# Optimization experiments

Measured on AMD Instinct MI355X. Metric: run time of the kernel, lower is better.

Reference implementation:

```python
import jax, jax.numpy as jnp
import numpy as np

MASK_SIZE = 28
IMG_H, IMG_W = 520, 704
NUM_GT = 128
NUM_PROP = 512


def box_iou(a, b):
    # a: [P,4], b: [G,4] in xyxy -> [P,G]
    area_a = (a[:, 2] - a[:, 0]) * (a[:, 3] - a[:, 1])
    area_b = (b[:, 2] - b[:, 0]) * (b[:, 3] - b[:, 1])
    lt = jnp.maximum(a[:, None, :2], b[None, :, :2])
    rb = jnp.minimum(a[:, None, 2:], b[None, :, 2:])
    wh = jnp.clip(rb - lt, 0.0)
    inter = wh[..., 0] * wh[..., 1]
    return inter / (area_a[:, None] + area_b[None, :] - inter)


def crop_resize_one(box, gidx, gt_masks):
    # Faithful to extract_mask_target: int-truncate box, clamp, crop, bilinear
    # resize (align_corners=False) to MASK_SIZE x MASK_SIZE.
    S = MASK_SIZE
    H, W = gt_masks.shape[1], gt_masks.shape[2]
    x1 = jnp.clip(box[0].astype(jnp.int32), 0, W - 1)
    y1 = jnp.clip(box[1].astype(jnp.int32), 0, H - 1)
    x2 = jnp.maximum(x1 + 1, jnp.minimum(box[2].astype(jnp.int32), W))
    y2 = jnp.maximum(y1 + 1, jnp.minimum(box[3].astype(jnp.int32), H))
    cwi = x2 - x1
    chi = y2 - y1
    cw = cwi.astype(jnp.float32)
    ch = chi.astype(jnp.float32)
    j = jnp.arange(S, dtype=jnp.float32)
    # source coords inside crop, border-clamped (PyTorch bilinear, align_corners=False)
    sx = jnp.clip((j + 0.5) * cw / S - 0.5, 0.0, cw - 1.0)
    sy = jnp.clip((j + 0.5) * ch / S - 0.5, 0.0, ch - 1.0)
    x0 = jnp.floor(sx)
    y0 = jnp.floor(sy)
    wx = sx - x0
    wy = sy - y0
    x0i = x0.astype(jnp.int32)
    y0i = y0.astype(jnp.int32)
    x1i = jnp.minimum(x0i + 1, cwi - 1)
    y1i = jnp.minimum(y0i + 1, chi - 1)
    m = gt_masks[gidx]  # [H, W]
    ax0 = x0i + x1
    ax1 = x1i + x1
    ay0 = y0i + y1
    ay1 = y1i + y1
    v00 = m[ay0[:, None], ax0[None, :]]
    v01 = m[ay0[:, None], ax1[None, :]]
    v10 = m[ay1[:, None], ax0[None, :]]
    v11 = m[ay1[:, None], ax1[None, :]]
    top = (1.0 - wx)[None, :] * v00 + wx[None, :] * v01
    bot = (1.0 - wx)[None, :] * v10 + wx[None, :] * v11
    return (1.0 - wy)[:, None] * top + wy[:, None] * bot  # [S, S]


def setup_inputs() -> dict:
    key = jax.random.key(0)
    k1, k2, k3, k4, k5 = jax.random.split(key, 5)
    # GT boxes: cell-like boxes inside a 520x704 image
    cx = jax.random.uniform(k1, (NUM_GT,), minval=50.0, maxval=IMG_W - 50.0)
    cy = jax.random.uniform(k2, (NUM_GT,), minval=50.0, maxval=IMG_H - 50.0)
    wh = jax.random.uniform(k3, (NUM_GT, 2), minval=20.0, maxval=80.0)
    gt_boxes = jnp.stack([cx - wh[:, 0] / 2, cy - wh[:, 1] / 2,
                          cx + wh[:, 0] / 2, cy + wh[:, 1] / 2], axis=1)
    # proposals: jittered copies of GT boxes -> realistic positive fraction
    reps = NUM_PROP // NUM_GT
    noise = jax.random.normal(k4, (NUM_PROP, 4)) * 4.0
    proposals = jnp.tile(gt_boxes, (reps, 1)) + noise
    # per-instance binary masks (float, as .float() in the torch code)
    gt_masks = (jax.random.uniform(k5, (NUM_GT, IMG_H, IMG_W)) < 0.3).astype(jnp.float32)
    mask_logits = jax.random.normal(jax.random.fold_in(key, 7),
                                    (NUM_PROP, 2, MASK_SIZE, MASK_SIZE), dtype=jnp.float32)
    return {"proposals": proposals, "gt_boxes": gt_boxes,
            "gt_masks": gt_masks, "mask_logits": mask_logits}


def reference(proposals, gt_boxes, gt_masks, mask_logits):
    S = MASK_SIZE
    ious = box_iou(proposals, gt_boxes)           # [P, G]
    max_ious = ious.max(axis=1)
    matched = jnp.argmax(ious, axis=1)            # [P]
    pos = (max_ious > 0.5).astype(jnp.float32)    # [P]
    matched_boxes = gt_boxes[matched]             # [P, 4]
    # batched crop + bilinear resize of matched GT masks (RoI-style gather)
    targets = jax.vmap(crop_resize_one, in_axes=(0, 0, None))(matched_boxes, matched, gt_masks)  # [P,S,S]
    logits = mask_logits[:, 1]                    # foreground channel [P,S,S]
    # stable BCE with logits
    bce = jnp.maximum(logits, 0.0) - logits * targets + jnp.log1p(jnp.exp(-jnp.abs(logits)))
    npos = pos.sum()
    loss_pos = jnp.sum(bce * pos[:, None, None]) / (jnp.maximum(npos, 1.0) * S * S)
    loss_neg = jnp.mean(mask_logits ** 2) * 0.01
    return jnp.where(npos > 0, loss_pos, loss_neg)
```

## Files before the change

kernel.cpp:

```cpp
#include <hip/hip_runtime.h>
#include <math.h>

#define NUM_GT   128
#define NUM_PROP 512
#define IMG_H    520
#define IMG_W    704
#define MS       28
#define LOGITS_N (NUM_PROP * 2 * MS * MS)

#define WS_MATCHED_OFF 256
#define WS_POS_OFF     (256 + NUM_PROP * 4)
#define WS_ZERO_BYTES  (256 + NUM_PROP * 8)

__global__ void match_kernel(const float* __restrict__ proposals,
                             const float* __restrict__ gt_boxes,
                             int* __restrict__ matched,
                             float* __restrict__ pos,
                             float* __restrict__ npos) {
    __shared__ float gb[NUM_GT * 4];
    for (int i = threadIdx.x; i < NUM_GT * 4; i += blockDim.x) gb[i] = gt_boxes[i];
    __syncthreads();

    int p = blockIdx.x * blockDim.x + threadIdx.x;
    if (p >= NUM_PROP) return;

    float ax1 = proposals[p * 4 + 0];
    float ay1 = proposals[p * 4 + 1];
    float ax2 = proposals[p * 4 + 2];
    float ay2 = proposals[p * 4 + 3];
    float area_a = (ax2 - ax1) * (ay2 - ay1);

    float best = -1e30f;
    int bi = 0;
    for (int g = 0; g < NUM_GT; ++g) {
        float bx1 = gb[g * 4 + 0];
        float by1 = gb[g * 4 + 1];
        float bx2 = gb[g * 4 + 2];
        float by2 = gb[g * 4 + 3];
        float area_b = (bx2 - bx1) * (by2 - by1);
        float ltx = fmaxf(ax1, bx1), lty = fmaxf(ay1, by1);
        float rbx = fminf(ax2, bx2), rby = fminf(ay2, by2);
        float w = fmaxf(rbx - ltx, 0.0f);
        float h = fmaxf(rby - lty, 0.0f);
        float inter = w * h;
        float iou = inter / (area_a + area_b - inter);
        if (iou > best) { best = iou; bi = g; }
    }
    matched[p] = bi;
    float ps = (best > 0.5f) ? 1.0f : 0.0f;
    pos[p] = ps;
    atomicAdd(npos, ps);
}

__global__ void bce_kernel(const float* __restrict__ gt_boxes,
                           const float* __restrict__ gt_masks,
                           const float* __restrict__ mask_logits,
                           const int* __restrict__ matched,
                           const float* __restrict__ pos,
                           float* __restrict__ bce_sum) {
    const int p = blockIdx.x;
    const int t = threadIdx.x;

    __shared__ int   s_gidx;
    __shared__ int   s_x0[MS], s_x1[MS], s_y0[MS], s_y1[MS];
    __shared__ float s_wx[MS], s_wy[MS];
    __shared__ float red[4];

    if (t == 0) s_gidx = matched[p];
    __syncthreads();
    const int g = s_gidx;

    const float b0 = gt_boxes[g * 4 + 0];
    const float b1 = gt_boxes[g * 4 + 1];
    const float b2 = gt_boxes[g * 4 + 2];
    const float b3 = gt_boxes[g * 4 + 3];

    int x1 = min(max((int)b0, 0), IMG_W - 1);
    int y1 = min(max((int)b1, 0), IMG_H - 1);
    int x2 = max(x1 + 1, min((int)b2, IMG_W));
    int y2 = max(y1 + 1, min((int)b3, IMG_H));
    int cwi = x2 - x1;
    int chi = y2 - y1;
    float cw = (float)cwi;
    float ch = (float)chi;

    if (t < MS) {
        float j = (float)t + 0.5f;
        float sx = fminf(fmaxf(j * cw / 28.0f - 0.5f, 0.0f), cw - 1.0f);
        float x0f = floorf(sx);
        int x0i = (int)x0f;
        s_wx[t] = sx - x0f;
        s_x0[t] = x0i + x1;
        s_x1[t] = min(x0i + 1, cwi - 1) + x1;

        float sy = fminf(fmaxf(j * ch / 28.0f - 0.5f, 0.0f), ch - 1.0f);
        float y0f = floorf(sy);
        int y0i = (int)y0f;
        s_wy[t] = sy - y0f;
        s_y0[t] = y0i + y1;
        s_y1[t] = min(y0i + 1, chi - 1) + y1;
    }
    __syncthreads();

    const float* m  = gt_masks + (size_t)g * IMG_H * IMG_W;
    const float* lg = mask_logits + ((size_t)p * 2 + 1) * (MS * MS);

    float acc = 0.0f;
    for (int idx = t; idx < MS * MS; idx += blockDim.x) {
        int i = idx / MS;
        int j = idx - i * MS;
        float wx = s_wx[j], wy = s_wy[i];
        const float* r0 = m + (size_t)s_y0[i] * IMG_W;
        const float* r1 = m + (size_t)s_y1[i] * IMG_W;
        int cx0 = s_x0[j], cx1 = s_x1[j];
        float v00 = r0[cx0], v01 = r0[cx1];
        float v10 = r1[cx0], v11 = r1[cx1];
        float top = (1.0f - wx) * v00 + wx * v01;
        float bot = (1.0f - wx) * v10 + wx * v11;
        float tv  = (1.0f - wy) * top + wy * bot;
        float l = lg[idx];
        float bce = fmaxf(l, 0.0f) - l * tv + log1pf(expf(-fabsf(l)));
        acc += bce;
    }

    float v = acc;
    #pragma unroll
    for (int o = 32; o > 0; o >>= 1) v += __shfl_down(v, o, 64);
    int lane = t & 63, wid = t >> 6;
    if (lane == 0) red[wid] = v;
    __syncthreads();
    if (t == 0) {
        float s = red[0] + red[1] + red[2] + red[3];
        atomicAdd(bce_sum, s * pos[p]);
    }
}

__global__ void sq_kernel(const float* __restrict__ mask_logits,
                          float* __restrict__ sqsum) {
    const int nvec = LOGITS_N / 4;
    const float4* src = (const float4*)mask_logits;
    float acc = 0.0f;
    for (int i = blockIdx.x * blockDim.x + threadIdx.x; i < nvec;
         i += gridDim.x * blockDim.x) {
        float4 x = src[i];
        acc += x.x * x.x + x.y * x.y + x.z * x.z + x.w * x.w;
    }
    float v = acc;
    #pragma unroll
    for (int o = 32; o > 0; o >>= 1) v += __shfl_down(v, o, 64);
    __shared__ float red[4];
    int lane = threadIdx.x & 63, wid = threadIdx.x >> 6;
    if (lane == 0) red[wid] = v;
    __syncthreads();
    if (threadIdx.x == 0) {
        float s = red[0] + red[1] + red[2] + red[3];
        atomicAdd(sqsum, s);
    }
}

__global__ void final_kernel(const float* __restrict__ acc, float* __restrict__ out) {
    float bce  = acc[0];
    float npos = acc[1];
    float sq   = acc[2];
    float loss_pos = bce / (fmaxf(npos, 1.0f) * (float)(MS * MS));
    float loss_neg = (sq / (float)LOGITS_N) * 0.01f;
    out[0] = (npos > 0.0f) ? loss_pos : loss_neg;
}

extern "C" void kernel_launch(void* const* d_in, const int* in_sizes, int n_in,
                              void* d_out, int out_size, void* d_ws, size_t ws_size,
                              hipStream_t stream) {
    const float* proposals   = (const float*)d_in[0];
    const float* gt_boxes    = (const float*)d_in[1];
    const float* gt_masks    = (const float*)d_in[2];
    const float* mask_logits = (const float*)d_in[3];
    float* out = (float*)d_out;

    float* acc     = (float*)d_ws;
    int*   matched = (int*)((char*)d_ws + WS_MATCHED_OFF);
    float* pos     = (float*)((char*)d_ws + WS_POS_OFF);

    hipMemsetAsync(d_ws, 0, WS_ZERO_BYTES, stream);

    match_kernel<<<(NUM_PROP + 255) / 256, 256, 0, stream>>>(proposals, gt_boxes,
                                                             matched, pos, acc + 1);
    bce_kernel<<<NUM_PROP, 256, 0, stream>>>(gt_boxes, gt_masks, mask_logits,
                                             matched, pos, acc + 0);
    sq_kernel<<<128, 256, 0, stream>>>(mask_logits, acc + 2);
    final_kernel<<<1, 1, 0, stream>>>(acc, out);
}
```

Before: 249.9 us.

## Fuse matching, BCE, square-sum and finalize into one kernel with last-block reduction

Merges the four kernels and the memset into a single launch. Each proposal block computes its IoU argmax cooperatively in shared memory, skips the mask gather and BCE for non-positive proposals, and extra blocks compute the squared-logit sum. The last block to finish, found through an atomic counter, writes the loss and resets the device-global accumulators. This removes launch overhead and the memset, at the cost of relying on global state reset between calls and a fence-based completion protocol.

```diff
diff --git a/kernel.cpp b/kernel.cpp
--- a/kernel.cpp
+++ b/kernel.cpp
@@ -7,185 +7,180 @@
 #define IMG_W    704
 #define MS       28
 #define LOGITS_N (NUM_PROP * 2 * MS * MS)
+#define SQ_BLOCKS 128
+#define TOTAL_BLOCKS (NUM_PROP + SQ_BLOCKS)
 
-#define WS_MATCHED_OFF 256
-#define WS_POS_OFF     (256 + NUM_PROP * 4)
-#define WS_ZERO_BYTES  (256 + NUM_PROP * 8)
+__device__ float    g_bce  = 0.0f;
+__device__ float    g_npos = 0.0f;
+__device__ float    g_sq   = 0.0f;
+__device__ unsigned g_done = 0u;
 
-__global__ void match_kernel(const float* __restrict__ proposals,
-                             const float* __restrict__ gt_boxes,
-                             int* __restrict__ matched,
-                             float* __restrict__ pos,
-                             float* __restrict__ npos) {
-    __shared__ float gb[NUM_GT * 4];
-    for (int i = threadIdx.x; i < NUM_GT * 4; i += blockDim.x) gb[i] = gt_boxes[i];
-    __syncthreads();
-
-    int p = blockIdx.x * blockDim.x + threadIdx.x;
-    if (p >= NUM_PROP) return;
-
-    float ax1 = proposals[p * 4 + 0];
-    float ay1 = proposals[p * 4 + 1];
-    float ax2 = proposals[p * 4 + 2];
-    float ay2 = proposals[p * 4 + 3];
-    float area_a = (ax2 - ax1) * (ay2 - ay1);
-
-    float best = -1e30f;
-    int bi = 0;
-    for (int g = 0; g < NUM_GT; ++g) {
-        float bx1 = gb[g * 4 + 0];
-        float by1 = gb[g * 4 + 1];
-        float bx2 = gb[g * 4 + 2];
-        float by2 = gb[g * 4 + 3];
-        float area_b = (bx2 - bx1) * (by2 - by1);
-        float ltx = fmaxf(ax1, bx1), lty = fmaxf(ay1, by1);
-        float rbx = fminf(ax2, bx2), rby = fminf(ay2, by2);
-        float w = fmaxf(rbx - ltx, 0.0f);
-        float h = fmaxf(rby - lty, 0.0f);
-        float inter = w * h;
-        float iou = inter / (area_a + area_b - inter);
-        if (iou > best) { best = iou; bi = g; }
-    }
-    matched[p] = bi;
-    float ps = (best > 0.5f) ? 1.0f : 0.0f;
-    pos[p] = ps;
-    atomicAdd(npos, ps);
-}
-
-__global__ void bce_kernel(const float* __restrict__ gt_boxes,
-                           const float* __restrict__ gt_masks,
-                           const float* __restrict__ mask_logits,
-                           const int* __restrict__ matched,
-                           const float* __restrict__ pos,
-                           float* __restrict__ bce_sum) {
-    const int p = blockIdx.x;
+__global__ __launch_bounds__(256) void fused_kernel(
+        const float* __restrict__ proposals,
+        const float* __restrict__ gt_boxes,
+        const float* __restrict__ gt_masks,
+        const float* __restrict__ mask_logits,
+        float* __restrict__ out)
+{
+    const int b = blockIdx.x;
     const int t = threadIdx.x;
 
-    __shared__ int   s_gidx;
-    __shared__ int   s_x0[MS], s_x1[MS], s_y0[MS], s_y1[MS];
-    __shared__ float s_wx[MS], s_wy[MS];
-    __shared__ float red[4];
+    if (b < NUM_PROP) {
+        const int p = b;
+        __shared__ float s_iou[NUM_GT];
+        __shared__ int   s_idx[NUM_GT];
+        __shared__ int   s_x0[MS], s_x1[MS], s_y0[MS], s_y1[MS];
+        __shared__ float s_wx[MS], s_wy[MS];
+        __shared__ float red[4];
 
-    if (t == 0) s_gidx = matched[p];
-    __syncthreads();
-    const int g = s_gidx;
+        const float ax1 = proposals[p * 4 + 0];
+        const float ay1 = proposals[p * 4 + 1];
+        const float ax2 = proposals[p * 4 + 2];
+        const float ay2 = proposals[p * 4 + 3];
+        const float area_a = (ax2 - ax1) * (ay2 - ay1);
 
-    const float b0 = gt_boxes[g * 4 + 0];
-    const float b1 = gt_boxes[g * 4 + 1];
-    const float b2 = gt_boxes[g * 4 + 2];
-    const float b3 = gt_boxes[g * 4 + 3];
+        if (t < NUM_GT) {
+            float bx1 = gt_boxes[t * 4 + 0];
+            float by1 = gt_boxes[t * 4 + 1];
+            float bx2 = gt_boxes[t * 4 + 2];
+            float by2 = gt_boxes[t * 4 + 3];
+            float area_b = (bx2 - bx1) * (by2 - by1);
+            float w = fmaxf(fminf(ax2, bx2) - fmaxf(ax1, bx1), 0.0f);
+            float h = fmaxf(fminf(ay2, by2) - fmaxf(ay1, by1), 0.0f);
+            float inter = w * h;
+            s_iou[t] = inter / (area_a + area_b - inter);
+            s_idx[t] = t;
+        }
+        __syncthreads();
 
-    int x1 = min(max((int)b0, 0), IMG_W - 1);
-    int y1 = min(max((int)b1, 0), IMG_H - 1);
-    int x2 = max(x1 + 1, min((int)b2, IMG_W));
-    int y2 = max(y1 + 1, min((int)b3, IMG_H));
-    int cwi = x2 - x1;
-    int chi = y2 - y1;
-    float cw = (float)cwi;
-    float ch = (float)chi;
+        for (int s = NUM_GT / 2; s > 0; s >>= 1) {
+            if (t < s) {
+                float a = s_iou[t], c = s_iou[t + s];
+                int   ia = s_idx[t], ic = s_idx[t + s];
+                if (c > a || (c == a && ic < ia)) { s_iou[t] = c; s_idx[t] = ic; }
+            }
+            __syncthreads();
+        }
+        const float best = s_iou[0];
+        const int   g    = s_idx[0];
+        const float ps   = (best > 0.5f) ? 1.0f : 0.0f;
 
-    if (t < MS) {
-        float j = (float)t + 0.5f;
-        float sx = fminf(fmaxf(j * cw / 28.0f - 0.5f, 0.0f), cw - 1.0f);
-        float x0f = floorf(sx);
-        int x0i = (int)x0f;
-        s_wx[t] = sx - x0f;
-        s_x0[t] = x0i + x1;
-        s_x1[t] = min(x0i + 1, cwi - 1) + x1;
+        if (t == 0) atomicAdd(&g_npos, ps);
 
-        float sy = fminf(fmaxf(j * ch / 28.0f - 0.5f, 0.0f), ch - 1.0f);
-        float y0f = floorf(sy);
-        int y0i = (int)y0f;
-        s_wy[t] = sy - y0f;
-        s_y0[t] = y0i + y1;
-        s_y1[t] = min(y0i + 1, chi - 1) + y1;
-    }
-    __syncthreads();
+        if (ps != 0.0f) {
+            const float b0 = gt_boxes[g * 4 + 0];
+            const float b1 = gt_boxes[g * 4 + 1];
+            const float b2 = gt_boxes[g * 4 + 2];
+            const float b3 = gt_boxes[g * 4 + 3];
 
-    const float* m  = gt_masks + (size_t)g * IMG_H * IMG_W;
-    const float* lg = mask_logits + ((size_t)p * 2 + 1) * (MS * MS);
+            int x1 = min(max((int)b0, 0), IMG_W - 1);
+            int y1 = min(max((int)b1, 0), IMG_H - 1);
+            int x2 = max(x1 + 1, min((int)b2, IMG_W));
+            int y2 = max(y1 + 1, min((int)b3, IMG_H));
+            int cwi = x2 - x1;
+            int chi = y2 - y1;
+            float cw = (float)cwi;
+            float ch = (float)chi;
 
-    float acc = 0.0f;
-    for (int idx = t; idx < MS * MS; idx += blockDim.x) {
-        int i = idx / MS;
-        int j = idx - i * MS;
-        float wx = s_wx[j], wy = s_wy[i];
-        const float* r0 = m + (size_t)s_y0[i] * IMG_W;
-        const float* r1 = m + (size_t)s_y1[i] * IMG_W;
-        int cx0 = s_x0[j], cx1 = s_x1[j];
-        float v00 = r0[cx0], v01 = r0[cx1];
-        float v10 = r1[cx0], v11 = r1[cx1];
-        float top = (1.0f - wx) * v00 + wx * v01;
-        float bot = (1.0f - wx) * v10 + wx * v11;
-        float tv  = (1.0f - wy) * top + wy * bot;
-        float l = lg[idx];
-        float bce = fmaxf(l, 0.0f) - l * tv + log1pf(expf(-fabsf(l)));
-        acc += bce;
+            if (t < MS) {
+                float j = (float)t + 0.5f;
+                float sx = fminf(fmaxf(j * cw / 28.0f - 0.5f, 0.0f), cw - 1.0f);
+                float x0f = floorf(sx);
+                int x0i = (int)x0f;
+                s_wx[t] = sx - x0f;
+                s_x0[t] = x0i + x1;
+                s_x1[t] = min(x0i + 1, cwi - 1) + x1;
+
+                float sy = fminf(fmaxf(j * ch / 28.0f - 0.5f, 0.0f), ch - 1.0f);
+                float y0f = floorf(sy);
+                int y0i = (int)y0f;
+                s_wy[t] = sy - y0f;
+                s_y0[t] = y0i + y1;
+                s_y1[t] = min(y0i + 1, chi - 1) + y1;
+            }
+            __syncthreads();
+
+            const float* m  = gt_masks + (size_t)g * IMG_H * IMG_W;
+            const float* lg = mask_logits + ((size_t)p * 2 + 1) * (MS * MS);
+
+            float acc = 0.0f;
+            for (int idx = t; idx < MS * MS; idx += 256) {
+                int i = idx / MS;
+                int j = idx - i * MS;
+                float wx = s_wx[j], wy = s_wy[i];
+                const float* r0 = m + (size_t)s_y0[i] * IMG_W;
+                const float* r1 = m + (size_t)s_y1[i] * IMG_W;
+                int cx0 = s_x0[j], cx1 = s_x1[j];
+                float v00 = r0[cx0], v01 = r0[cx1];
+                float v10 = r1[cx0], v11 = r1[cx1];
+                float top = (1.0f - wx) * v00 + wx * v01;
+                float bot = (1.0f - wx) * v10 + wx * v11;
+                float tv  = (1.0f - wy) * top + wy * bot;
+                float l = lg[idx];
+                acc += fmaxf(l, 0.0f) - l * tv + log1pf(expf(-fabsf(l)));
+            }
+
+            float v = acc;
+            #pragma unroll
+            for (int o = 32; o > 0; o >>= 1) v += __shfl_down(v, o, 64);
+            int lane = t & 63, wid = t >> 6;
+            if (lane == 0) red[wid] = v;
+            __syncthreads();
+            if (t == 0) {
+                float s = red[0] + red[1] + red[2] + red[3];
+                atomicAdd(&g_bce, s * ps);
+            }
+        }
+    } else {
+        const int sb = b - NUM_PROP;
+        const int nvec = LOGITS_N / 4;
+        const float4* src = (const float4*)mask_logits;
+        float acc = 0.0f;
+        for (int i = sb * 256 + t; i < nvec; i += SQ_BLOCKS * 256) {
+            float4 x = src[i];
+            acc += x.x * x.x + x.y * x.y + x.z * x.z + x.w * x.w;
+        }
+        float v = acc;
+        #pragma unroll
+        for (int o = 32; o > 0; o >>= 1) v += __shfl_down(v, o, 64);
+        __shared__ float redq[4];
+        int lane = t & 63, wid = t >> 6;
+        if (lane == 0) redq[wid] = v;
+        __syncthreads();
+        if (t == 0) {
+            atomicAdd(&g_sq, redq[0] + redq[1] + redq[2] + redq[3]);
+        }
     }
 
-    float v = acc;
-    #pragma unroll
-    for (int o = 32; o > 0; o >>= 1) v += __shfl_down(v, o, 64);
-    int lane = t & 63, wid = t >> 6;
-    if (lane == 0) red[wid] = v;
-    __syncthreads();
     if (t == 0) {
-        float s = red[0] + red[1] + red[2] + red[3];
-        atomicAdd(bce_sum, s * pos[p]);
+        __threadfence();
+        unsigned prev = atomicAdd(&g_done, 1u);
+        if (prev == TOTAL_BLOCKS - 1) {
+            float bce  = atomicAdd(&g_bce,  0.0f);
+            float npos = atomicAdd(&g_npos, 0.0f);
+            float sq   = atomicAdd(&g_sq,   0.0f);
+            float loss_pos = bce / (fmaxf(npos, 1.0f) * (float)(MS * MS));
+            float loss_neg = (sq / (float)LOGITS_N) * 0.01f;
+            out[0] = (npos > 0.0f) ? loss_pos : loss_neg;
+            atomicExch(&g_bce,  0.0f);
+            atomicExch(&g_npos, 0.0f);
+            atomicExch(&g_sq,   0.0f);
+            __threadfence();
+            atomicExch(&g_done, 0u);
+        }
     }
-}
-
-__global__ void sq_kernel(const float* __restrict__ mask_logits,
-                          float* __restrict__ sqsum) {
-    const int nvec = LOGITS_N / 4;
-    const float4* src = (const float4*)mask_logits;
-    float acc = 0.0f;
-    for (int i = blockIdx.x * blockDim.x + threadIdx.x; i < nvec;
-         i += gridDim.x * blockDim.x) {
-        float4 x = src[i];
-        acc += x.x * x.x + x.y * x.y + x.z * x.z + x.w * x.w;
-    }
-    float v = acc;
-    #pragma unroll
-    for (int o = 32; o > 0; o >>= 1) v += __shfl_down(v, o, 64);
-    __shared__ float red[4];
-    int lane = threadIdx.x & 63, wid = threadIdx.x >> 6;
-    if (lane == 0) red[wid] = v;
-    __syncthreads();
-    if (threadIdx.x == 0) {
-        float s = red[0] + red[1] + red[2] + red[3];
-        atomicAdd(sqsum, s);
-    }
-}
-
-__global__ void final_kernel(const float* __restrict__ acc, float* __restrict__ out) {
-    float bce  = acc[0];
-    float npos = acc[1];
-    float sq   = acc[2];
-    float loss_pos = bce / (fmaxf(npos, 1.0f) * (float)(MS * MS));
-    float loss_neg = (sq / (float)LOGITS_N) * 0.01f;
-    out[0] = (npos > 0.0f) ? loss_pos : loss_neg;
 }
 
 extern "C" void kernel_launch(void* const* d_in, const int* in_sizes, int n_in,
                               void* d_out, int out_size, void* d_ws, size_t ws_size,
                               hipStream_t stream) {
+    (void)in_sizes; (void)n_in; (void)d_ws; (void)ws_size; (void)out_size;
     const float* proposals   = (const float*)d_in[0];
     const float* gt_boxes    = (const float*)d_in[1];
     const float* gt_masks    = (const float*)d_in[2];
     const float* mask_logits = (const float*)d_in[3];
     float* out = (float*)d_out;
 
-    float* acc     = (float*)d_ws;
-    int*   matched = (int*)((char*)d_ws + WS_MATCHED_OFF);
-    float* pos     = (float*)((char*)d_ws + WS_POS_OFF);
-
-    hipMemsetAsync(d_ws, 0, WS_ZERO_BYTES, stream);
-
-    match_kernel<<<(NUM_PROP + 255) / 256, 256, 0, stream>>>(proposals, gt_boxes,
-                                                             matched, pos, acc + 1);
-    bce_kernel<<<NUM_PROP, 256, 0, stream>>>(gt_boxes, gt_masks, mask_logits,
-                                             matched, pos, acc + 0);
-    sq_kernel<<<128, 256, 0, stream>>>(mask_logits, acc + 2);
-    final_kernel<<<1, 1, 0, stream>>>(acc, out);
+    fused_kernel<<<TOTAL_BLOCKS, 256, 0, stream>>>(proposals, gt_boxes, gt_masks,
+                                                   mask_logits, out);
 }
```

Result: faster. 241.7 us (-3.3%).
